# Kernel optimization log

Hardware: AMD Instinct MI355X
Metric: run time of the kernel (lower is better)

The kernel has to match this reference:

```python
import jax, jax.numpy as jnp
import numpy as np

D_MODEL = 1024
N_HEADS = 16
D_HEAD = D_MODEL // N_HEADS
WIN = 128        # local_window
HALF = WIN // 2  # 64
KW = 2 * WIN     # kv window length per block (half-left + block + half-right)


def setup_inputs() -> dict:
    key = jax.random.key(0)
    ks = jax.random.split(key, 6)
    B, L = 2, 8192
    s = 0.02
    return {
        "x": jax.random.normal(ks[0], (B, L, D_MODEL), dtype=jnp.float32),
        "wq": jax.random.normal(ks[1], (D_MODEL, D_MODEL), dtype=jnp.float32) * s,
        "wk": jax.random.normal(ks[2], (D_MODEL, D_MODEL), dtype=jnp.float32) * s,
        "wv": jax.random.normal(ks[3], (D_MODEL, D_MODEL), dtype=jnp.float32) * s,
        "wo": jax.random.normal(ks[4], (D_MODEL, D_MODEL), dtype=jnp.float32) * s,
        "bo": jax.random.normal(ks[5], (D_MODEL,), dtype=jnp.float32) * s,
    }


def _rotate_half(t):
    t1, t2 = jnp.split(t, 2, axis=-1)
    return jnp.concatenate([-t2, t1], axis=-1)


def _rope(L, dtype):
    inv_freq = 1.0 / (10000.0 ** (jnp.arange(0, D_HEAD, 2, dtype=jnp.float32) / D_HEAD))
    t = jnp.arange(L, dtype=jnp.float32)
    freqs = t[:, None] * inv_freq[None, :]          # [L, D_HEAD/2]
    emb = jnp.concatenate([freqs, freqs], axis=-1)  # [L, D_HEAD]
    return jnp.cos(emb).astype(dtype), jnp.sin(emb).astype(dtype)


def reference(x, wq, wk, wv, wo, bo):
    B, L, D = x.shape
    H, Dh = N_HEADS, D_HEAD
    # projections (torch Linear: x @ W.T)
    q = (x @ wq.T).reshape(B, L, H, Dh).transpose(0, 2, 1, 3)  # [B,H,L,Dh]
    k = (x @ wk.T).reshape(B, L, H, Dh).transpose(0, 2, 1, 3)
    v = (x @ wv.T).reshape(B, L, H, Dh).transpose(0, 2, 1, 3)
    cos, sin = _rope(L, x.dtype)                    # [L, Dh]
    q = q * cos + _rotate_half(q) * sin
    k = k * cos + _rotate_half(k) * sin
    nb = L // WIN
    starts = jnp.arange(nb) * WIN - HALF            # window start per block
    idx = starts[:, None] + jnp.arange(KW)          # [nb, KW] kv indices
    valid = (idx >= 0) & (idx < L)
    idxc = jnp.clip(idx, 0, L - 1)
    kw = k[:, :, idxc]                              # [B,H,nb,KW,Dh]
    vw = v[:, :, idxc]
    qb = q.reshape(B, H, nb, WIN, Dh)
    scores = jnp.einsum('bhnqd,bhnkd->bhnqk', qb, kw) / np.sqrt(Dh).astype(x.dtype)
    scores = jnp.where(valid[None, None, :, None, :], scores, -jnp.inf)
    attn = jax.nn.softmax(scores, axis=-1)
    out = jnp.einsum('bhnqk,bhnkd->bhnqd', attn, vw).reshape(B, H, L, Dh)
    out = out.transpose(0, 2, 1, 3).reshape(B, L, D)
    return out @ wo.T + bo
```

## Files before the change

### kernel.cpp

```cpp
#include <hip/hip_runtime.h>
#include <cstdint>
#include <math.h>

#define L_SEQ 8192
#define DM    1024
#define NQK   2048

typedef unsigned short u16;
typedef __bf16 bf16;
typedef bf16  bf16x8 __attribute__((ext_vector_type(8)));
typedef float f32x4  __attribute__((ext_vector_type(4)));

__device__ __forceinline__ u16 f2bf(float f) {
    unsigned u = __float_as_uint(f);
    u += 0x7fffu + ((u >> 16) & 1u);
    return (u16)(u >> 16);
}

__device__ __forceinline__ f32x4 mfma16(bf16x8 a, bf16x8 b, f32x4 c) {
    return __builtin_amdgcn_mfma_f32_16x16x32_bf16(a, b, c, 0, 0, 0);
}

__device__ __forceinline__ void gld_lds16(const u16* g, u16* l) {
    __builtin_amdgcn_global_load_lds((const __attribute__((address_space(1))) void*)g,
                                     (__attribute__((address_space(3))) void*)l,
                                     16, 0, 0);
}

__global__ void cvt_bf16(const float* __restrict__ src, u16* __restrict__ dst, int n8) {
    int i = blockIdx.x * 256 + threadIdx.x;
    if (i >= n8) return;
    const float4* s4 = (const float4*)src;
    float4 a = s4[2 * i], b = s4[2 * i + 1];
    union { uint4 u; u16 h[8]; } r;
    r.h[0] = f2bf(a.x); r.h[1] = f2bf(a.y); r.h[2] = f2bf(a.z); r.h[3] = f2bf(a.w);
    r.h[4] = f2bf(b.x); r.h[5] = f2bf(b.y); r.h[6] = f2bf(b.z); r.h[7] = f2bf(b.w);
    ((uint4*)dst)[i] = r.u;
}

__global__ void rope_tbl(float2* __restrict__ t) {
    int idx = blockIdx.x * 256 + threadIdx.x;
    int pos = idx >> 5, i = idx & 31;
    float invf = exp2f(-0.4152410118609191f * (float)i);
    float s, c;
    sincosf((float)pos * invf, &s, &c);
    t[idx] = make_float2(c, s);
}


#define QITER(U, WIMM, RD, ST) do {                                            \
    __builtin_amdgcn_s_waitcnt(WIMM);                                          \
    __builtin_amdgcn_sched_barrier(0);                                         \
    __builtin_amdgcn_s_barrier();                                              \
    __builtin_amdgcn_sched_barrier(0);                                         \
    if (RD) {                                                                  \
        _Pragma("unroll")                                                      \
        for (int m = 0; m < 8; m++)                                            \
            fA[(U + 1) & 1][m] = *(const bf16x8*)(SAs + ((U + 1) % 3) * 8192 + aBase + m * 512); \
        _Pragma("unroll")                                                      \
        for (int n = 0; n < 4; n++)                                            \
            fB[(U + 1) & 1][n] = *(const bf16x8*)(SBs + ((U + 1) % 3) * 4096 + bBase + n * 512); \
    }                                                                          \
    if (ST) {                                                                  \
        _Pragma("unroll")                                                      \
        for (int i = 0; i < 4; ++i)                                            \
            gld_lds16(gA[i] + (U + 3) * 32, ldsAt + (U % 3) * 8192 + i * 2048);\
        _Pragma("unroll")                                                      \
        for (int i = 0; i < 2; ++i)                                            \
            gld_lds16(gB[i] + (U + 3) * 32, ldsBt + (U % 3) * 4096 + i * 2048);\
    }                                                                          \
    __builtin_amdgcn_sched_barrier(0);                                         \
    __builtin_amdgcn_s_setprio(1);                                             \
    _Pragma("unroll")                                                          \
    for (int m = 0; m < 8; m++)                                                \
        _Pragma("unroll")                                                      \
        for (int n = 0; n < 4; n++)                                            \
            acc[m][n] = mfma16(fA[(U) & 1][m], fB[(U) & 1][n], acc[m][n]);     \
    __builtin_amdgcn_s_setprio(0);                                             \
    __builtin_amdgcn_sched_barrier(0);                                         \
} while (0)

#define K_LOOP_ALL()                                                           \
    QITER(0,0x0076,1,1);  QITER(1,0x0076,1,1);  QITER(2,0x0076,1,1);           \
    QITER(3,0x0076,1,1);  QITER(4,0x0076,1,1);  QITER(5,0x0076,1,1);           \
    QITER(6,0x0076,1,1);  QITER(7,0x0076,1,1);  QITER(8,0x0076,1,1);           \
    QITER(9,0x0076,1,1);  QITER(10,0x0076,1,1); QITER(11,0x0076,1,1);          \
    QITER(12,0x0076,1,1); QITER(13,0x0076,1,1); QITER(14,0x0076,1,1);          \
    QITER(15,0x0076,1,1); QITER(16,0x0076,1,1); QITER(17,0x0076,1,1);          \
    QITER(18,0x0076,1,1); QITER(19,0x0076,1,1); QITER(20,0x0076,1,1);          \
    QITER(21,0x0076,1,1); QITER(22,0x0076,1,1); QITER(23,0x0076,1,1);          \
    QITER(24,0x0076,1,1); QITER(25,0x0076,1,1); QITER(26,0x0076,1,1);          \
    QITER(27,0x0076,1,1); QITER(28,0x0076,1,1); QITER(29,0x0076,1,0);          \
    QITER(30,0x0070,1,0); QITER(31,0x0070,0,0)

#define GEMM_SETUP()                                                           \
    u16* SAs = smem;                                \
    u16* SBs = smem + 24576;                        \
    const int tid = threadIdx.x;                                               \
    const int lane = tid & 63, w = tid >> 6;                                   \
    const int wm = w >> 1, wn = w & 1;                                         \
    const int quad = lane >> 4, ln = lane & 15;                                \
    const u16* gA[4]; const u16* gB[2];                                        \
    _Pragma("unroll")                                                          \
    for (int i = 0; i < 4; ++i) {                                              \
        int s = i * 256 + tid;                                                 \
        int li = s >> 3, pc = s & 7, lc = pc ^ (li & 7);                       \
        int row = 2 * li + (lc >> 2), kc = lc & 3;                             \
        gA[i] = Ap + (size_t)(m0 + row) * DM + kc * 8;                         \
    }                                                                          \
    _Pragma("unroll")                                                          \
    for (int i = 0; i < 2; ++i) {                                              \
        int s = i * 256 + tid;                                                 \
        int li = s >> 3, pc = s & 7, lc = pc ^ (li & 7);                       \
        int row = 2 * li + (lc >> 2), kc = lc & 3;                             \
        gB[i] = Bp + (size_t)(n0 + row) * DM + kc * 8;                         \
    }                                                                          \
    u16* ldsAt = SAs + tid * 8;                                                \
    u16* ldsBt = SBs + tid * 8;                                                \
    const int l7  = (ln >> 1) & 7;                                             \
    const int pcq = ((ln & 1) * 4 + quad) ^ l7;                                \
    const int aBase = (wm * 64 + (ln >> 1)) * 64 + pcq * 8;                    \
    const int bBase = (wn * 32 + (ln >> 1)) * 64 + pcq * 8;                    \
    const f32x4 fz = {0.f, 0.f, 0.f, 0.f};                                     \
    f32x4 acc[8][4];                                                           \
    _Pragma("unroll")                                                          \
    for (int a = 0; a < 8; a++)                                                \
        _Pragma("unroll")                                                      \
        for (int b = 0; b < 4; b++) acc[a][b] = fz;                            \
    bf16x8 fA[2][8], fB[2][4];                                                 \
                              \
    _Pragma("unroll")                                                          \
    for (int t3 = 0; t3 < 3; ++t3) {                                           \
        _Pragma("unroll")                                                      \
        for (int i = 0; i < 4; ++i) gld_lds16(gA[i] + t3 * 32, ldsAt + t3 * 8192 + i * 2048); \
        _Pragma("unroll")                                                      \
        for (int i = 0; i < 2; ++i) gld_lds16(gB[i] + t3 * 32, ldsBt + t3 * 4096 + i * 2048); \
    }                                                                          \
    __builtin_amdgcn_s_waitcnt(0x0F7C);        \
    __builtin_amdgcn_s_barrier();                                              \
    __builtin_amdgcn_sched_barrier(0);                                         \
    _Pragma("unroll")                                                          \
    for (int m = 0; m < 8; m++) fA[0][m] = *(const bf16x8*)(SAs + aBase + m * 512); \
    _Pragma("unroll")                                                          \
    for (int n = 0; n < 4; n++) fB[0][n] = *(const bf16x8*)(SBs + bBase + n * 512)

__global__ __launch_bounds__(256, 2) void gemm_qkv_fused(
    const u16* __restrict__ X,
    const u16* __restrict__ W,
    const float2* __restrict__ rope,
    u16* __restrict__ Y,
    u16* __restrict__ Vt)
{
    __shared__ __align__(16) u16 smem[36864];

    const int o   = (int)blockIdx.x;
    const int xcd = o & 7;
    const int r   = o >> 3;
    const int st  = r >> 6;
    const int t   = r & 63;
    const int m0  = (xcd * 8 + (t & 7)) * 256;
    const int n0  = (st * 8 + (t >> 3)) * 128;

    const u16* Ap = X;
    const u16* Bp = W;
    GEMM_SETUP();
    K_LOOP_ALL();
    __syncthreads();

    if (n0 < 2048) {
        #pragma unroll
        for (int mt = 0; mt < 8; mt++)
            #pragma unroll
            for (int reg = 0; reg < 4; reg++) {
                int rg = (m0 + wm * 128 + mt * 16 + quad * 4 + reg) & (L_SEQ - 1);
                const float2* rp = rope + rg * 32;
                #pragma unroll
                for (int nt = 0; nt < 2; nt++) {
                    float2 cs = rp[nt * 16 + ln];
                    float x1 = acc[mt][nt][reg], x2 = acc[mt][nt + 2][reg];
                    acc[mt][nt][reg]     = x1 * cs.x - x2 * cs.y;
                    acc[mt][nt + 2][reg] = x2 * cs.x + x1 * cs.y;
                }
            }
        u16* Es = smem;
        #pragma unroll
        for (int mh = 0; mh < 2; mh++) {
            if (mh) __syncthreads();
            if (wm == mh) {
                #pragma unroll
                for (int mt = 0; mt < 8; mt++)
                    #pragma unroll
                    for (int nt = 0; nt < 4; nt++)
                        #pragma unroll
                        for (int reg = 0; reg < 4; reg++)
                            Es[(mt * 16 + quad * 4 + reg) * 136 + wn * 64 + nt * 16 + ln] =
                                f2bf(acc[mt][nt][reg]);
            }
            __syncthreads();
            #pragma unroll
            for (int i = 0; i < 8; i++) {
                int idx = i * 256 + tid;
                int row = idx >> 4, ch = (idx & 15) * 8;
                uint4 v = *(const uint4*)(Es + row * 136 + ch);
                *(uint4*)(Y + (size_t)(m0 + mh * 128 + row) * NQK + n0 + ch) = v;
            }
        }
    } else {
        u16* Es = smem;
        const int bb = m0 >> 13, seq0 = m0 & (L_SEQ - 1);
        #pragma unroll
        for (int rh = 0; rh < 2; rh++) {
            if (rh) __syncthreads();
            if (wm == rh) {
                #pragma unroll
                for (int mt = 0; mt < 8; mt++)
                    #pragma unroll
                    for (int nt = 0; nt < 4; nt++)
                        #pragma unroll
                        for (int reg = 0; reg < 4; reg++)
                            Es[(wn * 64 + nt * 16 + ln) * 136 + mt * 16 + quad * 4 + reg] =
                                f2bf(acc[mt][nt][reg]);
            }
            __syncthreads();
            #pragma unroll
            for (int i = 0; i < 8; i++) {
                int idx = i * 256 + tid;
                int dr = idx >> 4, ch = (idx & 15) * 8;
                int gc = n0 - 2048 + dr;
                uint4 v = *(const uint4*)(Es + dr * 136 + ch);
                *(uint4*)(Vt + (size_t)(bb * 1024 + gc) * L_SEQ + seq0 + rh * 128 + ch) = v;
            }
        }
    }
}

__global__ __launch_bounds__(256, 2) void gemm_oproj(
    const u16* __restrict__ A,
    const u16* __restrict__ Wo,
    const float* __restrict__ bias,
    float* __restrict__ Out)
{
    __shared__ __align__(16) u16 smem[36864];

    const int o   = (int)blockIdx.x;
    const int xcd = o & 7;
    const int t   = o >> 3;
    const int m0  = (xcd * 8 + (t & 7)) * 256;
    const int n0  = (t >> 3) * 128;

    const u16* Ap = A;
    const u16* Bp = Wo;
    GEMM_SETUP();
    K_LOOP_ALL();
    __syncthreads();

    float b4[4];
    #pragma unroll
    for (int nt = 0; nt < 4; nt++) b4[nt] = bias[n0 + wn * 64 + nt * 16 + ln];

    float* Ef = (float*)smem;
    #pragma unroll
    for (int mq = 0; mq < 4; mq++) {
        if (mq) __syncthreads();
        if (wm == (mq >> 1)) {
            #pragma unroll
            for (int mt = 0; mt < 4; mt++)
                #pragma unroll
                for (int nt = 0; nt < 4; nt++)
                    #pragma unroll
                    for (int reg = 0; reg < 4; reg++)
                        Ef[(mt * 16 + quad * 4 + reg) * 132 + wn * 64 + nt * 16 + ln] =
                            acc[(mq & 1) * 4 + mt][nt][reg] + b4[nt];
        }
        __syncthreads();
        #pragma unroll
        for (int i = 0; i < 8; i++) {
            int idx = i * 256 + tid;
            int row = idx >> 5, ch = (idx & 31) * 4;
            float4 v = *(const float4*)(Ef + row * 132 + ch);
            *(float4*)(Out + (size_t)(m0 + mq * 64 + row) * DM + n0 + ch) = v;
        }
    }
}

__global__ __launch_bounds__(512, 4) void attn(
    const u16* __restrict__ QK,
    const u16* __restrict__ Vt,
    u16* __restrict__ AO)
{
    __shared__ __align__(16) u16 Ks[256 * 64];
    __shared__ __align__(16) u16 Vs[64 * 256];
    __shared__ __align__(16) u16 pbuf[8][512];

    const int blk = blockIdx.x;
    const int h   = blockIdx.y;
    const int b   = blockIdx.z;
    const int tid = threadIdx.x;
    const int lane = tid & 63, w = tid >> 6;
    const int quad = lane >> 4, ln = lane & 15;
    const int wstart = blk * 128 - 64;
    const size_t bbase = (size_t)b * L_SEQ;

    const u16* Kg = QK + 1024 + h * 64;
    const u16* Vg = Vt + (size_t)(b * 1024 + h * 64) * L_SEQ;

    #pragma unroll
    for (int i = 0; i < 4; i++) {
        int c = i * 512 + tid;
        int row = c >> 3, cl = c & 7, cg = cl ^ (row & 7);
        int kr = wstart + row;
        kr = kr < 0 ? 0 : (kr > L_SEQ - 1 ? L_SEQ - 1 : kr);
        gld_lds16(Kg + (size_t)(bbase + kr) * NQK + cg * 8, Ks + c * 8);
    }
    #pragma unroll
    for (int i = 0; i < 4; i++) {
        int c = i * 512 + tid;
        int d = c >> 5, kc = c & 31, cg = kc ^ (d & 7);
        int key = wstart + cg * 8;
        key = key < 0 ? 0 : (key > L_SEQ - 8 ? L_SEQ - 8 : key);
        gld_lds16(Vg + (size_t)d * L_SEQ + key, Vs + c * 8);
    }

    const int qrow = blk * 128 + w * 16 + ln;
    const u16* qp = QK + (bbase + qrow) * NQK + h * 64 + quad * 8;
    bf16x8 aq0 = *(const bf16x8*)qp;
    bf16x8 aq1 = *(const bf16x8*)(qp + 32);
    __syncthreads();

    const f32x4 fz = {0.f, 0.f, 0.f, 0.f};
    f32x4 s[16];
    #pragma unroll
    for (int nt = 0; nt < 16; nt++) {
        int row = nt * 16 + ln;
        bf16x8 b0 = *(const bf16x8*)(Ks + row * 64 + ((quad       ^ (ln & 7)) * 8));
        bf16x8 b1 = *(const bf16x8*)(Ks + row * 64 + (((4 + quad) ^ (ln & 7)) * 8));
        f32x4 t = mfma16(aq0, b0, fz);
        t = mfma16(aq1, b1, t);
        s[nt] = t;
    }
    __syncthreads();

    const float SC = 0.125f * 1.4426950408889634f;
    float mr[4] = {-INFINITY, -INFINITY, -INFINITY, -INFINITY};
    #pragma unroll
    for (int nt = 0; nt < 16; nt++) {
        int key = wstart + nt * 16 + ln;
        bool valid = (key >= 0) && (key < L_SEQ);
        #pragma unroll
        for (int r = 0; r < 4; r++) {
            float v = valid ? s[nt][r] * SC : -INFINITY;
            s[nt][r] = v;
            mr[r] = fmaxf(mr[r], v);
        }
    }
    #pragma unroll
    for (int off = 1; off < 16; off <<= 1)
        #pragma unroll
        for (int r = 0; r < 4; r++) mr[r] = fmaxf(mr[r], __shfl_xor(mr[r], off));

    float lr[4] = {0.f, 0.f, 0.f, 0.f};
    #pragma unroll
    for (int nt = 0; nt < 16; nt++)
        #pragma unroll
        for (int r = 0; r < 4; r++) {
            float p = exp2f(s[nt][r] - mr[r]);
            s[nt][r] = p;
            lr[r] += p;
        }
    #pragma unroll
    for (int off = 1; off < 16; off <<= 1)
        #pragma unroll
        for (int r = 0; r < 4; r++) lr[r] += __shfl_xor(lr[r], off);
    float rl[4];
    #pragma unroll
    for (int r = 0; r < 4; r++) rl[r] = 1.f / lr[r];

    u16* pb = pbuf[w];
    f32x4 o[4] = {fz, fz, fz, fz};
    #pragma unroll
    for (int ks = 0; ks < 8; ks++) {
        #pragma unroll
        for (int n2 = 0; n2 < 2; n2++) {
            int nt = ks * 2 + n2;
            #pragma unroll
            for (int r = 0; r < 4; r++)
                pb[(quad * 4 + r) * 32 + ((n2 * 16 + ln) ^ (quad * 8))] = f2bf(s[nt][r]);
        }
        bf16x8 ap = *(const bf16x8*)(pb + ln * 32 + ((quad * 8) ^ (((ln >> 2) & 3) * 8)));
        #pragma unroll
        for (int dt = 0; dt < 4; dt++) {
            int d = dt * 16 + ln;
            bf16x8 vb = *(const bf16x8*)(Vs + d * 256 + (((ks * 4 + quad) ^ (ln & 7)) * 8));
            o[dt] = mfma16(ap, vb, o[dt]);
        }
    }

    u16* AOs = Ks;
    #pragma unroll
    for (int dt = 0; dt < 4; dt++)
        #pragma unroll
        for (int r = 0; r < 4; r++)
            AOs[(w * 16 + quad * 4 + r) * 72 + dt * 16 + ln] = f2bf(o[dt][r] * rl[r]);
    __syncthreads();
    #pragma unroll
    for (int i = 0; i < 2; i++) {
        int c = i * 512 + tid;
        int row = c >> 3, ch = (c & 7) * 8;
        uint4 v = *(const uint4*)(AOs + row * 72 + ch);
        *(uint4*)(AO + (bbase + blk * 128 + row) * DM + h * 64 + ch) = v;
    }
}

extern "C" void kernel_launch(void* const* d_in, const int* in_sizes, int n_in,
                              void* d_out, int out_size, void* d_ws, size_t ws_size,
                              hipStream_t stream) {
    const float* x  = (const float*)d_in[0];
    const float* wq = (const float*)d_in[1];
    const float* wk = (const float*)d_in[2];
    const float* wv = (const float*)d_in[3];
    const float* wo = (const float*)d_in[4];
    const float* bo = (const float*)d_in[5];
    float* out = (float*)d_out;

    char* ws = (char*)d_ws;
    const size_t MB = 1024 * 1024;
    u16*   xb  = (u16*)ws;
    u16*   fqk = (u16*)(ws + 32 * MB);
    u16*   vt  = (u16*)(ws + 96 * MB);
    u16*   wf  = (u16*)(ws + 128 * MB);
    float2* rt = (float2*)(ws + 134 * MB);
    u16*   wob = (u16*)(ws + 136 * MB);
    u16*   aob = xb;

    cvt_bf16<<<8192, 256, 0, stream>>>(x, xb, 2097152);
    cvt_bf16<<<512, 256, 0, stream>>>(wq, wf, 131072);
    cvt_bf16<<<512, 256, 0, stream>>>(wk, wf + 1024 * 1024, 131072);
    cvt_bf16<<<512, 256, 0, stream>>>(wv, wf + 2 * 1024 * 1024, 131072);
    cvt_bf16<<<512, 256, 0, stream>>>(wo, wob, 131072);
    rope_tbl<<<1024, 256, 0, stream>>>(rt);

    gemm_qkv_fused<<<1536, 256, 0, stream>>>(xb, wf, rt, fqk, vt);
    attn<<<dim3(64, 16, 2), 512, 0, stream>>>(fqk, vt, aob);
    gemm_oproj<<<512, 256, 0, stream>>>(aob, wob, bo, out);
}
```

Measured before the change: 365.7 us.

## Use 32x32x16 MFMA in QKV GEMM and merge weight/rope prep kernels

The QKV projection GEMM switches from 16x16x32 to 32x32x16 bf16 MFMA tiles. This remaps the LDS fragment reads, the accumulator layout, the RoPE epilogue and the store epilogue to the 32x32 output lane mapping. The four weight-conversion launches and the rope table launch are folded into one prep kernel to cut launch overhead. The larger MFMA tile means fewer instructions and LDS reads per FLOP, but it changes register pressure and the epilogue access pattern.

```diff
diff --git a/kernel.cpp b/kernel.cpp
--- a/kernel.cpp
+++ b/kernel.cpp
@@ -10,6 +10,7 @@
 typedef __bf16 bf16;
 typedef bf16  bf16x8 __attribute__((ext_vector_type(8)));
 typedef float f32x4  __attribute__((ext_vector_type(4)));
+typedef float f32x16 __attribute__((ext_vector_type(16)));
 
 __device__ __forceinline__ u16 f2bf(float f) {
     unsigned u = __float_as_uint(f);
@@ -19,6 +20,9 @@
 
 __device__ __forceinline__ f32x4 mfma16(bf16x8 a, bf16x8 b, f32x4 c) {
     return __builtin_amdgcn_mfma_f32_16x16x32_bf16(a, b, c, 0, 0, 0);
+}
+__device__ __forceinline__ f32x16 mfma32(bf16x8 a, bf16x8 b, f32x16 c) {
+    return __builtin_amdgcn_mfma_f32_32x32x16_bf16(a, b, c, 0, 0, 0);
 }
 
 __device__ __forceinline__ void gld_lds16(const u16* g, u16* l) {
@@ -38,68 +42,36 @@
     ((uint4*)dst)[i] = r.u;
 }
 
-__global__ void rope_tbl(float2* __restrict__ t) {
+__global__ void prep_misc(const float* __restrict__ wq, const float* __restrict__ wk,
+                          const float* __restrict__ wv, const float* __restrict__ wo,
+                          u16* __restrict__ wf, u16* __restrict__ wob,
+                          float2* __restrict__ rt) {
     int idx = blockIdx.x * 256 + threadIdx.x;
-    int pos = idx >> 5, i = idx & 31;
-    float invf = exp2f(-0.4152410118609191f * (float)i);
-    float s, c;
-    sincosf((float)pos * invf, &s, &c);
-    t[idx] = make_float2(c, s);
-}
-
-
-#define QITER(U, WIMM, RD, ST) do {                                            \
-    __builtin_amdgcn_s_waitcnt(WIMM);                                          \
-    __builtin_amdgcn_sched_barrier(0);                                         \
-    __builtin_amdgcn_s_barrier();                                              \
-    __builtin_amdgcn_sched_barrier(0);                                         \
-    if (RD) {                                                                  \
-        _Pragma("unroll")                                                      \
-        for (int m = 0; m < 8; m++)                                            \
-            fA[(U + 1) & 1][m] = *(const bf16x8*)(SAs + ((U + 1) % 3) * 8192 + aBase + m * 512); \
-        _Pragma("unroll")                                                      \
-        for (int n = 0; n < 4; n++)                                            \
-            fB[(U + 1) & 1][n] = *(const bf16x8*)(SBs + ((U + 1) % 3) * 4096 + bBase + n * 512); \
-    }                                                                          \
-    if (ST) {                                                                  \
-        _Pragma("unroll")                                                      \
-        for (int i = 0; i < 4; ++i)                                            \
-            gld_lds16(gA[i] + (U + 3) * 32, ldsAt + (U % 3) * 8192 + i * 2048);\
-        _Pragma("unroll")                                                      \
-        for (int i = 0; i < 2; ++i)                                            \
-            gld_lds16(gB[i] + (U + 3) * 32, ldsBt + (U % 3) * 4096 + i * 2048);\
-    }                                                                          \
-    __builtin_amdgcn_sched_barrier(0);                                         \
-    __builtin_amdgcn_s_setprio(1);                                             \
-    _Pragma("unroll")                                                          \
-    for (int m = 0; m < 8; m++)                                                \
-        _Pragma("unroll")                                                      \
-        for (int n = 0; n < 4; n++)                                            \
-            acc[m][n] = mfma16(fA[(U) & 1][m], fB[(U) & 1][n], acc[m][n]);     \
-    __builtin_amdgcn_s_setprio(0);                                             \
-    __builtin_amdgcn_sched_barrier(0);                                         \
-} while (0)
-
-#define K_LOOP_ALL()                                                           \
-    QITER(0,0x0076,1,1);  QITER(1,0x0076,1,1);  QITER(2,0x0076,1,1);           \
-    QITER(3,0x0076,1,1);  QITER(4,0x0076,1,1);  QITER(5,0x0076,1,1);           \
-    QITER(6,0x0076,1,1);  QITER(7,0x0076,1,1);  QITER(8,0x0076,1,1);           \
-    QITER(9,0x0076,1,1);  QITER(10,0x0076,1,1); QITER(11,0x0076,1,1);          \
-    QITER(12,0x0076,1,1); QITER(13,0x0076,1,1); QITER(14,0x0076,1,1);          \
-    QITER(15,0x0076,1,1); QITER(16,0x0076,1,1); QITER(17,0x0076,1,1);          \
-    QITER(18,0x0076,1,1); QITER(19,0x0076,1,1); QITER(20,0x0076,1,1);          \
-    QITER(21,0x0076,1,1); QITER(22,0x0076,1,1); QITER(23,0x0076,1,1);          \
-    QITER(24,0x0076,1,1); QITER(25,0x0076,1,1); QITER(26,0x0076,1,1);          \
-    QITER(27,0x0076,1,1); QITER(28,0x0076,1,1); QITER(29,0x0076,1,0);          \
-    QITER(30,0x0070,1,0); QITER(31,0x0070,0,0)
-
-#define GEMM_SETUP()                                                           \
-    u16* SAs = smem;                                \
-    u16* SBs = smem + 24576;                        \
+    if (idx < 524288) {
+        int sel = idx >> 17, i = idx & 131071;
+        const float* s = sel == 0 ? wq : sel == 1 ? wk : sel == 2 ? wv : wo;
+        u16* d        = sel == 0 ? wf : sel == 1 ? wf + 1048576 : sel == 2 ? wf + 2097152 : wob;
+        const float4* s4 = (const float4*)s;
+        float4 a = s4[2 * i], b = s4[2 * i + 1];
+        union { uint4 u; u16 h[8]; } r;
+        r.h[0] = f2bf(a.x); r.h[1] = f2bf(a.y); r.h[2] = f2bf(a.z); r.h[3] = f2bf(a.w);
+        r.h[4] = f2bf(b.x); r.h[5] = f2bf(b.y); r.h[6] = f2bf(b.z); r.h[7] = f2bf(b.w);
+        ((uint4*)d)[i] = r.u;
+    } else {
+        int j = idx - 524288;
+        int pos = j >> 5, i = j & 31;
+        float invf = exp2f(-0.4152410118609191f * (float)i);
+        float s, c;
+        sincosf((float)pos * invf, &s, &c);
+        rt[j] = make_float2(c, s);
+    }
+}
+
+
+#define STAGE_COMMON()                                                         \
     const int tid = threadIdx.x;                                               \
     const int lane = tid & 63, w = tid >> 6;                                   \
     const int wm = w >> 1, wn = w & 1;                                         \
-    const int quad = lane >> 4, ln = lane & 15;                                \
     const u16* gA[4]; const u16* gB[2];                                        \
     _Pragma("unroll")                                                          \
     for (int i = 0; i < 4; ++i) {                                              \
@@ -117,17 +89,6 @@
     }                                                                          \
     u16* ldsAt = SAs + tid * 8;                                                \
     u16* ldsBt = SBs + tid * 8;                                                \
-    const int l7  = (ln >> 1) & 7;                                             \
-    const int pcq = ((ln & 1) * 4 + quad) ^ l7;                                \
-    const int aBase = (wm * 64 + (ln >> 1)) * 64 + pcq * 8;                    \
-    const int bBase = (wn * 32 + (ln >> 1)) * 64 + pcq * 8;                    \
-    const f32x4 fz = {0.f, 0.f, 0.f, 0.f};                                     \
-    f32x4 acc[8][4];                                                           \
-    _Pragma("unroll")                                                          \
-    for (int a = 0; a < 8; a++)                                                \
-        _Pragma("unroll")                                                      \
-        for (int b = 0; b < 4; b++) acc[a][b] = fz;                            \
-    bf16x8 fA[2][8], fB[2][4];                                                 \
                               \
     _Pragma("unroll")                                                          \
     for (int t3 = 0; t3 < 3; ++t3) {                                           \
@@ -135,14 +96,53 @@
         for (int i = 0; i < 4; ++i) gld_lds16(gA[i] + t3 * 32, ldsAt + t3 * 8192 + i * 2048); \
         _Pragma("unroll")                                                      \
         for (int i = 0; i < 2; ++i) gld_lds16(gB[i] + t3 * 32, ldsBt + t3 * 4096 + i * 2048); \
-    }                                                                          \
-    __builtin_amdgcn_s_waitcnt(0x0F7C);        \
+    }
+
+#define QITER32(U, WIMM, RD, ST) do {                                          \
+    __builtin_amdgcn_s_waitcnt(WIMM);                                          \
     __builtin_amdgcn_s_barrier();                                              \
     __builtin_amdgcn_sched_barrier(0);                                         \
+    if (RD) {                                                                  \
+        _Pragma("unroll")                                                      \
+        for (int mt = 0; mt < 4; mt++) {                                       \
+            fA[(U + 1) & 1][mt][0] = *(const bf16x8*)(SAs + ((U + 1) % 3) * 8192 + aB + mt * 1024 + pc0 * 8); \
+            fA[(U + 1) & 1][mt][1] = *(const bf16x8*)(SAs + ((U + 1) % 3) * 8192 + aB + mt * 1024 + pc1 * 8); \
+        }                                                                      \
+        _Pragma("unroll")                                                      \
+        for (int nt = 0; nt < 2; nt++) {                                       \
+            fB[(U + 1) & 1][nt][0] = *(const bf16x8*)(SBs + ((U + 1) % 3) * 4096 + bB + nt * 1024 + pc0 * 8); \
+            fB[(U + 1) & 1][nt][1] = *(const bf16x8*)(SBs + ((U + 1) % 3) * 4096 + bB + nt * 1024 + pc1 * 8); \
+        }                                                                      \
+    }                                                                          \
+    if (ST) {                                                                  \
+        _Pragma("unroll")                                                      \
+        for (int i = 0; i < 4; ++i)                                            \
+            gld_lds16(gA[i] + (U + 3) * 32, ldsAt + (U % 3) * 8192 + i * 2048);\
+        _Pragma("unroll")                                                      \
+        for (int i = 0; i < 2; ++i)                                            \
+            gld_lds16(gB[i] + (U + 3) * 32, ldsBt + (U % 3) * 4096 + i * 2048);\
+    }                                                                          \
     _Pragma("unroll")                                                          \
-    for (int m = 0; m < 8; m++) fA[0][m] = *(const bf16x8*)(SAs + aBase + m * 512); \
-    _Pragma("unroll")                                                          \
-    for (int n = 0; n < 4; n++) fB[0][n] = *(const bf16x8*)(SBs + bBase + n * 512)
+    for (int s = 0; s < 2; s++)                                                \
+        _Pragma("unroll")                                                      \
+        for (int mt = 0; mt < 4; mt++)                                         \
+            _Pragma("unroll")                                                  \
+            for (int nt = 0; nt < 2; nt++)                                     \
+                acc[mt][nt] = mfma32(fA[(U) & 1][mt][s], fB[(U) & 1][nt][s], acc[mt][nt]); \
+} while (0)
+
+#define K_LOOP32()                                                             \
+    QITER32(0,0x0076,1,1);  QITER32(1,0x0076,1,1);  QITER32(2,0x0076,1,1);     \
+    QITER32(3,0x0076,1,1);  QITER32(4,0x0076,1,1);  QITER32(5,0x0076,1,1);     \
+    QITER32(6,0x0076,1,1);  QITER32(7,0x0076,1,1);  QITER32(8,0x0076,1,1);     \
+    QITER32(9,0x0076,1,1);  QITER32(10,0x0076,1,1); QITER32(11,0x0076,1,1);    \
+    QITER32(12,0x0076,1,1); QITER32(13,0x0076,1,1); QITER32(14,0x0076,1,1);    \
+    QITER32(15,0x0076,1,1); QITER32(16,0x0076,1,1); QITER32(17,0x0076,1,1);    \
+    QITER32(18,0x0076,1,1); QITER32(19,0x0076,1,1); QITER32(20,0x0076,1,1);    \
+    QITER32(21,0x0076,1,1); QITER32(22,0x0076,1,1); QITER32(23,0x0076,1,1);    \
+    QITER32(24,0x0076,1,1); QITER32(25,0x0076,1,1); QITER32(26,0x0076,1,1);    \
+    QITER32(27,0x0076,1,1); QITER32(28,0x0076,1,1); QITER32(29,0x0076,1,0);    \
+    QITER32(30,0x0070,1,0); QITER32(31,0x0070,0,0)
 
 __global__ __launch_bounds__(256, 2) void gemm_qkv_fused(
     const u16* __restrict__ X,
@@ -152,6 +152,8 @@
     u16* __restrict__ Vt)
 {
     __shared__ __align__(16) u16 smem[36864];
+    u16* SAs = smem;
+    u16* SBs = smem + 24576;
 
     const int o   = (int)blockIdx.x;
     const int xcd = o & 7;
@@ -163,24 +165,52 @@
 
     const u16* Ap = X;
     const u16* Bp = W;
-    GEMM_SETUP();
-    K_LOOP_ALL();
+    STAGE_COMMON();
+
+    const int l31 = lane & 31, hi = lane >> 5;
+    const int l2  = l31 >> 1;
+    const int p4  = (lane & 1) * 4;
+    const int pc0 = (p4 + hi) ^ (l2 & 7);
+    const int pc1 = (p4 + 2 + hi) ^ (l2 & 7);
+    const int aB  = wm * 4096 + l2 * 64;
+    const int bB  = wn * 2048 + l2 * 64;
+
+    const f32x16 fz16 = {0.f,0.f,0.f,0.f,0.f,0.f,0.f,0.f,0.f,0.f,0.f,0.f,0.f,0.f,0.f,0.f};
+    f32x16 acc[4][2];
+    #pragma unroll
+    for (int a = 0; a < 4; a++)
+        #pragma unroll
+        for (int b = 0; b < 2; b++) acc[a][b] = fz16;
+    bf16x8 fA[2][4][2], fB[2][2][2];
+
+    __builtin_amdgcn_s_waitcnt(0x0F7C);
+    __builtin_amdgcn_s_barrier();
+    __builtin_amdgcn_sched_barrier(0);
+    #pragma unroll
+    for (int mt = 0; mt < 4; mt++) {
+        fA[0][mt][0] = *(const bf16x8*)(SAs + aB + mt * 1024 + pc0 * 8);
+        fA[0][mt][1] = *(const bf16x8*)(SAs + aB + mt * 1024 + pc1 * 8);
+    }
+    #pragma unroll
+    for (int nt = 0; nt < 2; nt++) {
+        fB[0][nt][0] = *(const bf16x8*)(SBs + bB + nt * 1024 + pc0 * 8);
+        fB[0][nt][1] = *(const bf16x8*)(SBs + bB + nt * 1024 + pc1 * 8);
+    }
+
+    K_LOOP32();
     __syncthreads();
 
     if (n0 < 2048) {
         #pragma unroll
-        for (int mt = 0; mt < 8; mt++)
+        for (int mt = 0; mt < 4; mt++)
             #pragma unroll
-            for (int reg = 0; reg < 4; reg++) {
-                int rg = (m0 + wm * 128 + mt * 16 + quad * 4 + reg) & (L_SEQ - 1);
-                const float2* rp = rope + rg * 32;
-                #pragma unroll
-                for (int nt = 0; nt < 2; nt++) {
-                    float2 cs = rp[nt * 16 + ln];
-                    float x1 = acc[mt][nt][reg], x2 = acc[mt][nt + 2][reg];
-                    acc[mt][nt][reg]     = x1 * cs.x - x2 * cs.y;
-                    acc[mt][nt + 2][reg] = x2 * cs.x + x1 * cs.y;
-                }
+            for (int reg = 0; reg < 16; reg++) {
+                int crr = (reg & 3) + 8 * (reg >> 2) + 4 * hi;
+                int rg = (m0 + wm * 128 + mt * 32 + crr) & (L_SEQ - 1);
+                float2 cs = rope[rg * 32 + l31];
+                float x1 = acc[mt][0][reg], x2 = acc[mt][1][reg];
+                acc[mt][0][reg] = x1 * cs.x - x2 * cs.y;
+                acc[mt][1][reg] = x2 * cs.x + x1 * cs.y;
             }
         u16* Es = smem;
         #pragma unroll
@@ -188,13 +218,15 @@
             if (mh) __syncthreads();
             if (wm == mh) {
                 #pragma unroll
-                for (int mt = 0; mt < 8; mt++)
+                for (int mt = 0; mt < 4; mt++)
                     #pragma unroll
-                    for (int nt = 0; nt < 4; nt++)
+                    for (int nt = 0; nt < 2; nt++)
                         #pragma unroll
-                        for (int reg = 0; reg < 4; reg++)
-                            Es[(mt * 16 + quad * 4 + reg) * 136 + wn * 64 + nt * 16 + ln] =
+                        for (int reg = 0; reg < 16; reg++) {
+                            int crr = (reg & 3) + 8 * (reg >> 2) + 4 * hi;
+                            Es[(mt * 32 + crr) * 136 + wn * 64 + nt * 32 + l31] =
                                 f2bf(acc[mt][nt][reg]);
+                        }
             }
             __syncthreads();
             #pragma unroll
@@ -213,13 +245,15 @@
             if (rh) __syncthreads();
             if (wm == rh) {
                 #pragma unroll
-                for (int mt = 0; mt < 8; mt++)
+                for (int mt = 0; mt < 4; mt++)
                     #pragma unroll
-                    for (int nt = 0; nt < 4; nt++)
+                    for (int nt = 0; nt < 2; nt++)
                         #pragma unroll
-                        for (int reg = 0; reg < 4; reg++)
-                            Es[(wn * 64 + nt * 16 + ln) * 136 + mt * 16 + quad * 4 + reg] =
+                        for (int reg = 0; reg < 16; reg++) {
+                            int crr = (reg & 3) + 8 * (reg >> 2) + 4 * hi;
+                            Es[(wn * 64 + nt * 32 + l31) * 136 + mt * 32 + crr] =
                                 f2bf(acc[mt][nt][reg]);
+                        }
             }
             __syncthreads();
             #pragma unroll
@@ -234,6 +268,51 @@
     }
 }
 
+#define QITER(U, WIMM, RD, ST) do {                                            \
+    __builtin_amdgcn_s_waitcnt(WIMM);                                          \
+    __builtin_amdgcn_sched_barrier(0);                                         \
+    __builtin_amdgcn_s_barrier();                                              \
+    __builtin_amdgcn_sched_barrier(0);                                         \
+    if (RD) {                                                                  \
+        _Pragma("unroll")                                                      \
+        for (int m = 0; m < 8; m++)                                            \
+            fA[(U + 1) & 1][m] = *(const bf16x8*)(SAs + ((U + 1) % 3) * 8192 + aBase + m * 512); \
+        _Pragma("unroll")                                                      \
+        for (int n = 0; n < 4; n++)                                            \
+            fB[(U + 1) & 1][n] = *(const bf16x8*)(SBs + ((U + 1) % 3) * 4096 + bBase + n * 512); \
+    }                                                                          \
+    if (ST) {                                                                  \
+        _Pragma("unroll")                                                      \
+        for (int i = 0; i < 4; ++i)                                            \
+            gld_lds16(gA[i] + (U + 3) * 32, ldsAt + (U % 3) * 8192 + i * 2048);\
+        _Pragma("unroll")                                                      \
+        for (int i = 0; i < 2; ++i)                                            \
+            gld_lds16(gB[i] + (U + 3) * 32, ldsBt + (U % 3) * 4096 + i * 2048);\
+    }                                                                          \
+    __builtin_amdgcn_sched_barrier(0);                                         \
+    __builtin_amdgcn_s_setprio(1);                                             \
+    _Pragma("unroll")                                                          \
+    for (int m = 0; m < 8; m++)                                                \
+        _Pragma("unroll")                                                      \
+        for (int n = 0; n < 4; n++)                                            \
+            acc[m][n] = mfma16(fA[(U) & 1][m], fB[(U) & 1][n], acc[m][n]);     \
+    __builtin_amdgcn_s_setprio(0);                                             \
+    __builtin_amdgcn_sched_barrier(0);                                         \
+} while (0)
+
+#define K_LOOP_ALL()                                                           \
+    QITER(0,0x0076,1,1);  QITER(1,0x0076,1,1);  QITER(2,0x0076,1,1);           \
+    QITER(3,0x0076,1,1);  QITER(4,0x0076,1,1);  QITER(5,0x0076,1,1);           \
+    QITER(6,0x0076,1,1);  QITER(7,0x0076,1,1);  QITER(8,0x0076,1,1);           \
+    QITER(9,0x0076,1,1);  QITER(10,0x0076,1,1); QITER(11,0x0076,1,1);          \
+    QITER(12,0x0076,1,1); QITER(13,0x0076,1,1); QITER(14,0x0076,1,1);          \
+    QITER(15,0x0076,1,1); QITER(16,0x0076,1,1); QITER(17,0x0076,1,1);          \
+    QITER(18,0x0076,1,1); QITER(19,0x0076,1,1); QITER(20,0x0076,1,1);          \
+    QITER(21,0x0076,1,1); QITER(22,0x0076,1,1); QITER(23,0x0076,1,1);          \
+    QITER(24,0x0076,1,1); QITER(25,0x0076,1,1); QITER(26,0x0076,1,1);          \
+    QITER(27,0x0076,1,1); QITER(28,0x0076,1,1); QITER(29,0x0076,1,0);          \
+    QITER(30,0x0070,1,0); QITER(31,0x0070,0,0)
+
 __global__ __launch_bounds__(256, 2) void gemm_oproj(
     const u16* __restrict__ A,
     const u16* __restrict__ Wo,
@@ -241,6 +320,8 @@
     float* __restrict__ Out)
 {
     __shared__ __align__(16) u16 smem[36864];
+    u16* SAs = smem;
+    u16* SBs = smem + 24576;
 
     const int o   = (int)blockIdx.x;
     const int xcd = o & 7;
@@ -250,7 +331,30 @@
 
     const u16* Ap = A;
     const u16* Bp = Wo;
-    GEMM_SETUP();
+    STAGE_COMMON();
+
+    const int quad = lane >> 4, ln = lane & 15;
+    const int l7  = (ln >> 1) & 7;
+    const int pcq = ((ln & 1) * 4 + quad) ^ l7;
+    const int aBase = (wm * 64 + (ln >> 1)) * 64 + pcq * 8;
+    const int bBase = (wn * 32 + (ln >> 1)) * 64 + pcq * 8;
+
+    const f32x4 fz = {0.f, 0.f, 0.f, 0.f};
+    f32x4 acc[8][4];
+    #pragma unroll
+    for (int a = 0; a < 8; a++)
+        #pragma unroll
+        for (int b = 0; b < 4; b++) acc[a][b] = fz;
+    bf16x8 fA[2][8], fB[2][4];
+
+    __builtin_amdgcn_s_waitcnt(0x0F7C);
+    __builtin_amdgcn_s_barrier();
+    __builtin_amdgcn_sched_barrier(0);
+    #pragma unroll
+    for (int m = 0; m < 8; m++) fA[0][m] = *(const bf16x8*)(SAs + aBase + m * 512);
+    #pragma unroll
+    for (int n = 0; n < 4; n++) fB[0][n] = *(const bf16x8*)(SBs + bBase + n * 512);
+
     K_LOOP_ALL();
     __syncthreads();
 
@@ -433,11 +537,7 @@
     u16*   aob = xb;
 
     cvt_bf16<<<8192, 256, 0, stream>>>(x, xb, 2097152);
-    cvt_bf16<<<512, 256, 0, stream>>>(wq, wf, 131072);
-    cvt_bf16<<<512, 256, 0, stream>>>(wk, wf + 1024 * 1024, 131072);
-    cvt_bf16<<<512, 256, 0, stream>>>(wv, wf + 2 * 1024 * 1024, 131072);
-    cvt_bf16<<<512, 256, 0, stream>>>(wo, wob, 131072);
-    rope_tbl<<<1024, 256, 0, stream>>>(rt);
+    prep_misc<<<3072, 256, 0, stream>>>(wq, wk, wv, wo, wf, wob, rt);
 
     gemm_qkv_fused<<<1536, 256, 0, stream>>>(xb, wf, rt, fqk, vt);
     attn<<<dim3(64, 16, 2), 512, 0, stream>>>(fqk, vt, aob);
```

New measurement: 367.9 us. About the same (+0.6%).
